# Performance work log

Measured on AMD Instinct MI355X. Metric: run time of the kernel, lower is better.

## Reference

```python
import jax, jax.numpy as jnp
import numpy as np

N_ORDER = 64
PRED_LEN = 720
SEQ_LEN = 720
ENC_IN = 321
BATCH = 16


def _hippo_legs(N):
    # HiPPO-LegS continuous transition (A, B), float64 numpy
    q = np.arange(N, dtype=np.float64)
    col, row = np.meshgrid(q, q)
    r = 2.0 * q + 1.0
    M = -(np.where(row >= col, r, 0.0) - np.diag(q))
    T = np.sqrt(np.diag(2.0 * q + 1.0))
    A = T @ M @ np.linalg.inv(T)
    B = np.diag(T)[:, None].copy()
    return A, B


def _discretize_bilinear(A, B, dt):
    # scipy.signal.cont2discrete(..., method='bilinear') equivalent
    N = A.shape[0]
    I = np.eye(N)
    BL = np.linalg.inv(I - (dt / 2.0) * A)
    Ad = BL @ (I + (dt / 2.0) * A)
    Bd = (BL @ (dt * B)).squeeze(-1)
    return Ad, Bd


def _legendre_eval_matrix(N, dt):
    # ss.eval_legendre(np.arange(N)[:,None], 1 - 2*vals).T via 3-term recurrence
    vals = np.arange(0.0, 1.0, dt)
    x = 1.0 - 2.0 * vals
    Ps = [np.ones_like(x), x]
    for n in range(1, N - 1):
        Ps.append(((2.0 * n + 1.0) * x * Ps[-1] - n * Ps[-2]) / (n + 1.0))
    return np.stack(Ps[:N], axis=0).T  # [len(vals), N]


def setup_inputs() -> dict:
    key = jax.random.key(0)
    k1, k2, k3 = jax.random.split(key, 3)
    dt = 1.0 / PRED_LEN
    A, B = _hippo_legs(N_ORDER)
    Ad, Bd = _discretize_bilinear(A, B, dt)
    eval_matrix = _legendre_eval_matrix(N_ORDER, dt)
    bound = 1.0 / np.sqrt(N_ORDER)  # torch nn.Linear default init range
    return {
        "x_enc": jax.random.normal(k1, (BATCH, SEQ_LEN, ENC_IN), dtype=jnp.float32),
        "A": jnp.asarray(Ad, dtype=jnp.float32),
        "B_vec": jnp.asarray(Bd, dtype=jnp.float32),
        "eval_matrix": jnp.asarray(eval_matrix, dtype=jnp.float32),
        "W_mlp": jax.random.uniform(k2, (N_ORDER, N_ORDER), jnp.float32, -bound, bound),
        "b_mlp": jax.random.uniform(k3, (N_ORDER,), jnp.float32, -bound, bound),
        "affine_weight": jnp.ones((1, 1, ENC_IN), jnp.float32),
        "affine_bias": jnp.zeros((1, 1, ENC_IN), jnp.float32),
    }


def reference(x_enc, A, B_vec, eval_matrix, W_mlp, b_mlp, affine_weight, affine_bias):
    P, N = eval_matrix.shape  # pred_len, proj_degree

    # RevIN-style instance normalization (means/stdev detached in torch)
    means = jax.lax.stop_gradient(jnp.mean(x_enc, axis=1, keepdims=True))
    x = x_enc - means
    stdev = jax.lax.stop_gradient(jnp.sqrt(jnp.var(x, axis=1, keepdims=True) + 1e-5))
    x = x / stdev
    x = x * affine_weight + affine_bias

    x_in = x[:, -P:]                         # [B, P, E]
    xs = jnp.transpose(x_in, (1, 0, 2))      # [P, B, E]: time-major for scan
    c0 = jnp.zeros((x_in.shape[0], x_in.shape[2], N), x_enc.dtype)

    def step(c, f):
        # c_t = c_{t-1} @ A^T + f_t B  (HiPPO-LegS linear recurrence)
        c_new = c @ A.T + f[..., None] * B_vec
        return c_new, c_new

    _, cs = jax.lax.scan(step, c0, xs)       # [P, B, E, N]

    out1 = cs @ W_mlp.T + b_mlp              # mlp over coefficient dim N
    x_dec_c = out1[P - 1]                    # [B, E, N] (seq_len >= pred_len branch)
    x_dec = x_dec_c @ eval_matrix.T          # [B, E, P] Legendre reconstruction
    x_dec = jnp.transpose(x_dec, (0, 2, 1))  # [B, P, E]

    # de-normalize
    x_dec = (x_dec - affine_bias) / (affine_weight + 1e-10)
    x_dec = x_dec * stdev + means
    return x_dec
```

## Files before the change

### kernel.cpp

```cpp
#include <hip/hip_runtime.h>
#include <math.h>

#define BATCH 16
#define SEQ   720
#define ENC   321
#define NORD  64
#define PRED  720
#define NPAIR (BATCH*ENC)

#define WS_KT    0
#define WS_EWT   (WS_KT + PRED*NORD)
#define WS_EVB   (WS_EWT + NORD*PRED)
#define WS_A64   (WS_EVB + PRED)
#define WS_KSUMP (WS_A64 + 4096)
#define WS_G     (WS_KSUMP + 17*64)
#define WS_PSUM  (WS_G + 4*96*4096)
#define WS_PSS   (WS_PSUM + 4*16*6*64)

__global__ __launch_bounds__(256, 1) void prep2(const float* __restrict__ evalm,
        const float* __restrict__ W, const float* __restrict__ bm,
        const float* __restrict__ A, const float* __restrict__ Bv,
        float* __restrict__ ws)
{
    __shared__ float dsm[12800];
    const int tid  = threadIdx.x;
    const int lane = tid & 63;
    const int wv   = tid >> 6;
    if (blockIdx.x < 12) {
        float* smW = dsm;
        float* Et  = dsm + 4160;
        const int r = blockIdx.x;
        for (int idx = tid; idx < 4096; idx += 256)
            smW[(idx>>6)*65 + (idx&63)] = W[idx];
        __syncthreads();
        float bv = bm[lane];
        #pragma unroll
        for (int k = 0; k < 15; k++) {
            int row = wv + k*4;
            int tp = r*60 + row;
            const float* ev = evalm + (size_t)tp*64;
            float acc = 0.f;
            #pragma unroll
            for (int kk = 0; kk < 16; kk++) {
                float4 e4 = *(const float4*)&ev[4*kk];
                acc += e4.x*smW[(4*kk+0)*65+lane] + e4.y*smW[(4*kk+1)*65+lane]
                     + e4.z*smW[(4*kk+2)*65+lane] + e4.w*smW[(4*kk+3)*65+lane];
            }
            Et[lane*61 + row] = acc;
            float pv = ev[lane] * bv;
            #pragma unroll
            for (int o = 32; o > 0; o >>= 1) pv += __shfl_down(pv, o);
            if (lane == 0) ws[WS_EVB + tp] = pv;
        }
        __syncthreads();
        for (int idx = tid; idx < 4096; idx += 256) {
            int m = idx >> 6, row = idx & 63;
            if (row < 60)
                ws[WS_EWT + (size_t)m*720 + r*60 + row] = Et[m*61 + row];
        }
    } else {
        float* Kl  = dsm;
        float* Ap  = dsm + 4096;
        float* ApT = dsm + 8448;
        float* Kt  = ws + WS_KT;
        for (int idx = tid; idx < 4096; idx += 256) {
            int n = idx >> 6, m = idx & 63;
            float v = A[idx];
            Ap[n*68+m] = v; ApT[m*68+n] = v;
        }
        float ksml = 0.f;
        if (tid < 64) {
            float bv = Bv[tid];
            Kl[tid] = bv;
            Kt[(size_t)719*64 + tid] = bv;
            ksml += bv;
        }
        __syncthreads();
        float ar[64];
        #pragma unroll
        for (int k = 0; k < 16; k++) {
            float4 v = *(const float4*)&Ap[lane*68 + 4*k];
            ar[4*k]=v.x; ar[4*k+1]=v.y; ar[4*k+2]=v.z; ar[4*k+3]=v.w;
        }
        for (int mm = 1; mm <= 32; mm <<= 1) {
            for (int j2 = mm + wv; j2 < 2*mm; j2 += 4) {
                const float* src = &Kl[(j2 - mm)*64];
                float acc = 0.f;
                #pragma unroll
                for (int k = 0; k < 16; k++) {
                    float4 s = *(const float4*)&src[4*k];
                    acc += ar[4*k]*s.x + ar[4*k+1]*s.y + ar[4*k+2]*s.z + ar[4*k+3]*s.w;
                }
                Kl[j2*64 + lane] = acc;
                Kt[(size_t)(719 - j2)*64 + lane] = acc;
                ksml += acc;
            }
            float nacc[16];
            #pragma unroll
            for (int q = 0; q < 16; q++) {
                int c = wv*16 + q;
                const float* src = &ApT[c*68];
                float acc = 0.f;
                #pragma unroll
                for (int k = 0; k < 16; k++) {
                    float4 s = *(const float4*)&src[4*k];
                    acc += ar[4*k]*s.x + ar[4*k+1]*s.y + ar[4*k+2]*s.z + ar[4*k+3]*s.w;
                }
                nacc[q] = acc;
            }
            __syncthreads();
            #pragma unroll
            for (int q = 0; q < 16; q++) {
                int c = wv*16 + q;
                Ap[lane*68 + c]  = nacc[q];
                ApT[c*68 + lane] = nacc[q];
            }
            __syncthreads();
            #pragma unroll
            for (int k = 0; k < 16; k++) {
                float4 v = *(const float4*)&Ap[lane*68 + 4*k];
                ar[4*k]=v.x; ar[4*k+1]=v.y; ar[4*k+2]=v.z; ar[4*k+3]=v.w;
            }
        }
        for (int idx = tid; idx < 4096; idx += 256)
            ws[WS_A64 + idx] = Ap[(idx>>6)*68 + (idx&63)];
        __syncthreads();
        Kl[wv*64 + lane] = ksml;
        __syncthreads();
        if (tid < 64)
            ws[WS_KSUMP + 16*64 + tid] = Kl[tid] + Kl[64+tid] + Kl[128+tid] + Kl[192+tid];
    }
}

__global__ __launch_bounds__(256, 1) void chains(float* __restrict__ ws)
{
    __shared__ float sv[4][64];
    __shared__ float red[4][64];
    const int tid  = threadIdx.x;
    const int lane = tid & 63;
    const int wv   = tid >> 6;
    const int r    = blockIdx.x*4 + wv;
    const float* A64 = ws + WS_A64;
    float* Kt = ws + WS_KT;
    float ar64[64];
    #pragma unroll
    for (int k = 0; k < 16; k++) {
        float4 v = *(const float4*)&A64[lane*64 + 4*k];
        ar64[4*k]=v.x; ar64[4*k+1]=v.y; ar64[4*k+2]=v.z; ar64[4*k+3]=v.w;
    }
    float ksml = 0.f;
    sv[wv][lane] = Kt[(size_t)(719 - r)*64 + lane];
    for (int j = r + 64; j <= 719; j += 64) {
        float acc = 0.f;
        #pragma unroll
        for (int k = 0; k < 16; k++) {
            float4 v = *(const float4*)&sv[wv][4*k];
            acc += ar64[4*k]*v.x + ar64[4*k+1]*v.y + ar64[4*k+2]*v.z + ar64[4*k+3]*v.w;
        }
        sv[wv][lane] = acc;
        Kt[(size_t)(719 - j)*64 + lane] = acc;
        ksml += acc;
    }
    red[wv][lane] = ksml;
    __syncthreads();
    if (tid < 64)
        ws[WS_KSUMP + blockIdx.x*64 + tid] = red[0][tid] + red[1][tid] + red[2][tid] + red[3][tid];
}

__device__ inline float4 ldx(const float* __restrict__ x, int b, int t, int e4)
{
    float4 r = make_float4(0.f,0.f,0.f,0.f);
    const float* p = x + ((size_t)b*SEQ + t)*ENC;
    if (e4 + 3 < ENC) r = *(const float4*)&p[e4];
    else {
        if (e4   < ENC) r.x = p[e4];
        if (e4+1 < ENC) r.y = p[e4+1];
        if (e4+2 < ENC) r.z = p[e4+2];
    }
    return r;
}

__global__ __launch_bounds__(256) void k2(const float* __restrict__ x,
        float* __restrict__ ws)
{
    __shared__ float xt[2][12*64];
    __shared__ float ks[2][12*64];
    __shared__ float redn[12*64];
    __shared__ float reds[12*64];
    const int tid = threadIdx.x;
    const int bid = blockIdx.x;
    const int b = bid / 24, rem = bid % 24;
    const int et = rem / 4, tsp = rem % 4;
    const int e0 = et*64, t0 = tsp*180;

    const bool xon = tid < 192;
    const bool kon = tid >= 64;
    const int sx_t  = tid >> 4;
    const int sx_e4 = (tid & 15) * 4;
    const int sk    = tid - 64;
    const int sk_t  = sk >> 4;
    const int sk_m4 = (sk & 15) * 4;

    const float* Kt = ws + WS_KT;
    float s0=0,s1=0,s2=0,s3=0, q0=0,q1=0,q2=0,q3=0;
    float4 rx = make_float4(0,0,0,0), rk = make_float4(0,0,0,0);

    if (xon) rx = ldx(x, b, t0 + sx_t, e0 + sx_e4);
    if (kon) rk = *(const float4*)&Kt[(size_t)(t0 + sk_t)*64 + sk_m4];
    if (xon) {
        *(float4*)&xt[0][sx_t*64 + sx_e4] = rx;
        s0+=rx.x; s1+=rx.y; s2+=rx.z; s3+=rx.w;
        q0+=rx.x*rx.x; q1+=rx.y*rx.y; q2+=rx.z*rx.z; q3+=rx.w*rx.w;
    }
    if (kon) *(float4*)&ks[0][sk_t*64 + sk_m4] = rk;

    const int lane = tid & 63, wv = tid >> 6;
    const int elg = lane & 15;
    const int mgr = wv*4 + (lane >> 4);
    float acc[4][4];
    #pragma unroll
    for (int j = 0; j < 4; j++)
        #pragma unroll
        for (int i = 0; i < 4; i++) acc[j][i] = 0.f;

    for (int ch = 0; ch < 15; ch++) {
        if (ch + 1 < 15) {
            if (xon) rx = ldx(x, b, t0 + (ch+1)*12 + sx_t, e0 + sx_e4);
            if (kon) rk = *(const float4*)&Kt[(size_t)(t0 + (ch+1)*12 + sk_t)*64 + sk_m4];
        }
        __syncthreads();
        const float* xb = xt[ch & 1];
        const float* kb = ks[ch & 1];
        #pragma unroll
        for (int tt = 0; tt < 12; tt++) {
            float4 f  = *(const float4*)&xb[tt*64 + elg*4];
            float4 kv = *(const float4*)&kb[tt*64 + mgr*4];
            acc[0][0]+=f.x*kv.x; acc[0][1]+=f.x*kv.y; acc[0][2]+=f.x*kv.z; acc[0][3]+=f.x*kv.w;
            acc[1][0]+=f.y*kv.x; acc[1][1]+=f.y*kv.y; acc[1][2]+=f.y*kv.z; acc[1][3]+=f.y*kv.w;
            acc[2][0]+=f.z*kv.x; acc[2][1]+=f.z*kv.y; acc[2][2]+=f.z*kv.z; acc[2][3]+=f.z*kv.w;
            acc[3][0]+=f.w*kv.x; acc[3][1]+=f.w*kv.y; acc[3][2]+=f.w*kv.z; acc[3][3]+=f.w*kv.w;
        }
        if (ch + 1 < 15) {
            if (xon) {
                *(float4*)&xt[(ch+1)&1][sx_t*64 + sx_e4] = rx;
                s0+=rx.x; s1+=rx.y; s2+=rx.z; s3+=rx.w;
                q0+=rx.x*rx.x; q1+=rx.y*rx.y; q2+=rx.z*rx.z; q3+=rx.w*rx.w;
            }
            if (kon) *(float4*)&ks[(ch+1)&1][sk_t*64 + sk_m4] = rk;
        }
    }

    float* g = ws + WS_G + (size_t)(tsp*96 + b*6 + et)*4096;
    #pragma unroll
    for (int i = 0; i < 4; i++)
        *(float4*)&g[(mgr*4 + i)*64 + elg*4] =
            make_float4(acc[0][i], acc[1][i], acc[2][i], acc[3][i]);

    __syncthreads();
    if (xon) {
        redn[sx_t*64 + sx_e4+0] = s0; redn[sx_t*64 + sx_e4+1] = s1;
        redn[sx_t*64 + sx_e4+2] = s2; redn[sx_t*64 + sx_e4+3] = s3;
        reds[sx_t*64 + sx_e4+0] = q0; reds[sx_t*64 + sx_e4+1] = q1;
        reds[sx_t*64 + sx_e4+2] = q2; reds[sx_t*64 + sx_e4+3] = q3;
    }
    __syncthreads();
    if (tid < 64) {
        float s = 0.f, q = 0.f;
        #pragma unroll
        for (int rr = 0; rr < 12; rr++) { s += redn[rr*64 + tid]; q += reds[rr*64 + tid]; }
        const size_t o = (size_t)((tsp*16 + b)*6 + et)*64 + tid;
        ws[WS_PSUM + o] = s;
        ws[WS_PSS  + o] = q;
    }
}

__global__ __launch_bounds__(256) void k3f(const float* __restrict__ aw,
        const float* __restrict__ ab, const float* __restrict__ ws,
        float* __restrict__ out)
{
    __shared__ float Cm[64*132];
    __shared__ float EWm[64*68];
    __shared__ float ssc[128], ssh[128], smean[128], ssd[128], siaw[128], sabe[128];
    __shared__ float kss[64];
    const int tid = threadIdx.x;
    const int b   = blockIdx.x / 12;
    const int rr  = blockIdx.x % 12;
    const int eT  = rr / 4;
    const int tq  = rr % 4;
    const int e0  = eT * 128;
    const int et0 = eT * 2;

    if (tid < 128) {
        const int el = tid, e = e0 + el;
        const int et = et0 + (el >> 6), eli = el & 63;
        float s = 0.f, q = 0.f;
        #pragma unroll
        for (int tsp = 0; tsp < 4; tsp++) {
            const size_t o = (size_t)((tsp*16 + b)*6 + et)*64 + eli;
            s += ws[WS_PSUM + o];
            q += ws[WS_PSS  + o];
        }
        float mean = s * (1.0f/SEQ);
        float var  = q * (1.0f/SEQ) - mean*mean;
        float sd   = sqrtf(var + 1e-5f);
        if (e < ENC) {
            float a = aw[e], av = ab[e];
            float sc = a / sd;
            ssc[el] = sc; ssh[el] = av - mean*sc;
            smean[el] = mean; ssd[el] = sd;
            siaw[el] = 1.0f/(a + 1e-10f); sabe[el] = av;
        } else {
            ssc[el]=0.f; ssh[el]=0.f; smean[el]=0.f; ssd[el]=0.f; siaw[el]=0.f; sabe[el]=0.f;
        }
    }
    if (tid < 64) {
        float s = 0.f;
        #pragma unroll
        for (int p = 0; p < 17; p++) s += ws[WS_KSUMP + p*64 + tid];
        kss[tid] = s;
    }
    __syncthreads();

    const float* G = ws + WS_G;
    #pragma unroll
    for (int k = 0; k < 8; k++) {
        int slot = k*256 + tid;
        int m = slot >> 5, el4 = (slot & 31) * 4;
        int et = et0 + (el4 >> 6), eli4 = el4 & 63;
        size_t base = (size_t)(b*6 + et)*4096 + m*64 + eli4;
        float4 g0 = *(const float4*)&G[base];
        float4 g1 = *(const float4*)&G[base + (size_t) 96*4096];
        float4 g2 = *(const float4*)&G[base + (size_t)192*4096];
        float4 g3 = *(const float4*)&G[base + (size_t)288*4096];
        float km = kss[m];
        float4 c;
        c.x = ssc[el4+0]*(g0.x+g1.x+g2.x+g3.x) + ssh[el4+0]*km;
        c.y = ssc[el4+1]*(g0.y+g1.y+g2.y+g3.y) + ssh[el4+1]*km;
        c.z = ssc[el4+2]*(g0.z+g1.z+g2.z+g3.z) + ssh[el4+2]*km;
        c.w = ssc[el4+3]*(g0.w+g1.w+g2.w+g3.w) + ssh[el4+3]*km;
        *(float4*)&Cm[m*132 + el4] = c;
    }
    __syncthreads();

    const float* EWT = ws + WS_EWT;
    const float* evb = ws + WS_EVB;
    const int tx = tid & 31;
    const int ty = tid >> 5;
    for (int ti = 0; ti < 3; ti++) {
        const int tt0 = (tq*3 + ti) * 64;
        if (ti > 0) __syncthreads();
        #pragma unroll
        for (int k = 0; k < 4; k++) {
            int slot = k*256 + tid;
            int m = slot >> 4, t4 = (slot & 15)*4;
            int tp = tt0 + t4;
            float4 v;
            if (tp + 3 < PRED) v = *(const float4*)&EWT[(size_t)m*720 + tp];
            else {
                v = make_float4(0.f,0.f,0.f,0.f);
                if (tp   < PRED) v.x = EWT[(size_t)m*720 + tp];
                if (tp+1 < PRED) v.y = EWT[(size_t)m*720 + tp+1];
                if (tp+2 < PRED) v.z = EWT[(size_t)m*720 + tp+2];
            }
            *(float4*)&EWm[m*68 + t4] = v;
        }
        __syncthreads();

        float acc[8][4];
        #pragma unroll
        for (int i = 0; i < 8; i++)
            #pragma unroll
            for (int j = 0; j < 4; j++) acc[i][j] = 0.f;

        #pragma unroll 4
        for (int m = 0; m < 64; m++) {
            float4 c4 = *(const float4*)&Cm[m*132 + tx*4];
            float4 w0 = *(const float4*)&EWm[m*68 + ty*8];
            float4 w1 = *(const float4*)&EWm[m*68 + ty*8 + 4];
            acc[0][0]+=w0.x*c4.x; acc[0][1]+=w0.x*c4.y; acc[0][2]+=w0.x*c4.z; acc[0][3]+=w0.x*c4.w;
            acc[1][0]+=w0.y*c4.x; acc[1][1]+=w0.y*c4.y; acc[1][2]+=w0.y*c4.z; acc[1][3]+=w0.y*c4.w;
            acc[2][0]+=w0.z*c4.x; acc[2][1]+=w0.z*c4.y; acc[2][2]+=w0.z*c4.z; acc[2][3]+=w0.z*c4.w;
            acc[3][0]+=w0.w*c4.x; acc[3][1]+=w0.w*c4.y; acc[3][2]+=w0.w*c4.z; acc[3][3]+=w0.w*c4.w;
            acc[4][0]+=w1.x*c4.x; acc[4][1]+=w1.x*c4.y; acc[4][2]+=w1.x*c4.z; acc[4][3]+=w1.x*c4.w;
            acc[5][0]+=w1.y*c4.x; acc[5][1]+=w1.y*c4.y; acc[5][2]+=w1.y*c4.z; acc[5][3]+=w1.y*c4.w;
            acc[6][0]+=w1.z*c4.x; acc[6][1]+=w1.z*c4.y; acc[6][2]+=w1.z*c4.z; acc[6][3]+=w1.z*c4.w;
            acc[7][0]+=w1.w*c4.x; acc[7][1]+=w1.w*c4.y; acc[7][2]+=w1.w*c4.z; acc[7][3]+=w1.w*c4.w;
        }

        const int elb = tx*4;
        const int ebase = e0 + elb;
        #pragma unroll
        for (int i = 0; i < 8; i++) {
            int tp = tt0 + ty*8 + i;
            if (tp < PRED) {
                float ev = evb[tp];
                float* op = out + ((size_t)b*PRED + tp)*ENC;
                #pragma unroll
                for (int j = 0; j < 4; j++) {
                    int e = ebase + j;
                    if (e < ENC)
                        op[e] = (acc[i][j] + ev - sabe[elb+j]) * siaw[elb+j] * ssd[elb+j]
                                + smean[elb+j];
                }
            }
        }
    }
}

extern "C" void kernel_launch(void* const* d_in, const int* in_sizes, int n_in,
                              void* d_out, int out_size, void* d_ws, size_t ws_size,
                              hipStream_t stream)
{
    const float* x     = (const float*)d_in[0];
    const float* A     = (const float*)d_in[1];
    const float* Bv    = (const float*)d_in[2];
    const float* evalm = (const float*)d_in[3];
    const float* W     = (const float*)d_in[4];
    const float* bm    = (const float*)d_in[5];
    const float* aw    = (const float*)d_in[6];
    const float* ab    = (const float*)d_in[7];
    float* ws  = (float*)d_ws;
    float* out = (float*)d_out;

    prep2 <<<13, 256, 0, stream>>>(evalm, W, bm, A, Bv, ws);
    chains<<<16, 256, 0, stream>>>(ws);
    k2    <<<BATCH*6*4, 256, 0, stream>>>(x, ws);
    k3f   <<<192, 256, 0, stream>>>(aw, ab, ws, out);
}
```

Baseline: 178.2 us.

## Rebalance Krylov power precompute: fewer matrix squarings, longer stride-16 chains

```diff
diff --git a/kernel.cpp b/kernel.cpp
--- a/kernel.cpp
+++ b/kernel.cpp
@@ -11,25 +11,130 @@
 #define WS_KT    0
 #define WS_EWT   (WS_KT + PRED*NORD)
 #define WS_EVB   (WS_EWT + NORD*PRED)
-#define WS_A64   (WS_EVB + PRED)
-#define WS_KSUMP (WS_A64 + 4096)
+#define WS_A16   (WS_EVB + PRED)
+#define WS_KSUMP (WS_A16 + 4096)
 #define WS_G     (WS_KSUMP + 17*64)
 #define WS_PSUM  (WS_G + 4*96*4096)
 #define WS_PSS   (WS_PSUM + 4*16*6*64)
 
-__global__ __launch_bounds__(256, 1) void prep2(const float* __restrict__ evalm,
-        const float* __restrict__ W, const float* __restrict__ bm,
-        const float* __restrict__ A, const float* __restrict__ Bv,
-        float* __restrict__ ws)
-{
-    __shared__ float dsm[12800];
+__global__ __launch_bounds__(256, 1) void prepK(const float* __restrict__ A,
+        const float* __restrict__ Bv, float* __restrict__ ws)
+{
+    __shared__ float Kl[16*64];
+    __shared__ float Ap[64*68];
+    __shared__ float ApT[64*68];
+    __shared__ float red[4*64];
     const int tid  = threadIdx.x;
     const int lane = tid & 63;
     const int wv   = tid >> 6;
-    if (blockIdx.x < 12) {
+    float* Kt = ws + WS_KT;
+    for (int idx = tid; idx < 4096; idx += 256) {
+        int n = idx >> 6, m = idx & 63;
+        float v = A[idx];
+        Ap[n*68+m] = v; ApT[m*68+n] = v;
+    }
+    float ksml = 0.f;
+    if (tid < 64) {
+        float bv = Bv[tid];
+        Kl[tid] = bv;
+        Kt[(size_t)719*64 + tid] = bv;
+        ksml += bv;
+    }
+    __syncthreads();
+    float ar[64];
+    #pragma unroll
+    for (int k = 0; k < 16; k++) {
+        float4 v = *(const float4*)&Ap[lane*68 + 4*k];
+        ar[4*k]=v.x; ar[4*k+1]=v.y; ar[4*k+2]=v.z; ar[4*k+3]=v.w;
+    }
+    for (int mm = 1; mm <= 8; mm <<= 1) {
+        for (int j2 = mm + wv; j2 < 2*mm; j2 += 4) {
+            const float* src = &Kl[(j2 - mm)*64];
+            float acc = 0.f;
+            #pragma unroll
+            for (int k = 0; k < 16; k++) {
+                float4 s = *(const float4*)&src[4*k];
+                acc += ar[4*k]*s.x + ar[4*k+1]*s.y + ar[4*k+2]*s.z + ar[4*k+3]*s.w;
+            }
+            Kl[j2*64 + lane] = acc;
+            Kt[(size_t)(719 - j2)*64 + lane] = acc;
+            ksml += acc;
+        }
+        float nacc[16];
+        #pragma unroll
+        for (int q = 0; q < 16; q++) {
+            int c = wv*16 + q;
+            const float* src = &ApT[c*68];
+            float acc = 0.f;
+            #pragma unroll
+            for (int k = 0; k < 16; k++) {
+                float4 s = *(const float4*)&src[4*k];
+                acc += ar[4*k]*s.x + ar[4*k+1]*s.y + ar[4*k+2]*s.z + ar[4*k+3]*s.w;
+            }
+            nacc[q] = acc;
+        }
+        __syncthreads();
+        #pragma unroll
+        for (int q = 0; q < 16; q++) {
+            int c = wv*16 + q;
+            Ap[lane*68 + c]  = nacc[q];
+            ApT[c*68 + lane] = nacc[q];
+        }
+        __syncthreads();
+        #pragma unroll
+        for (int k = 0; k < 16; k++) {
+            float4 v = *(const float4*)&Ap[lane*68 + 4*k];
+            ar[4*k]=v.x; ar[4*k+1]=v.y; ar[4*k+2]=v.z; ar[4*k+3]=v.w;
+        }
+        mm = mm;
+    }
+    for (int idx = tid; idx < 4096; idx += 256)
+        ws[WS_A16 + idx] = Ap[(idx>>6)*68 + (idx&63)];
+    __syncthreads();
+    red[wv*64 + lane] = ksml;
+    __syncthreads();
+    if (tid < 64)
+        ws[WS_KSUMP + 16*64 + tid] = red[tid] + red[64+tid] + red[128+tid] + red[192+tid];
+}
+
+__global__ __launch_bounds__(256, 1) void chainsEW(const float* __restrict__ evalm,
+        const float* __restrict__ W, const float* __restrict__ bm,
+        float* __restrict__ ws)
+{
+    __shared__ float dsm[8224];
+    const int tid  = threadIdx.x;
+    const int lane = tid & 63;
+    const int wv   = tid >> 6;
+    if (blockIdx.x < 16) {
+        if (tid >= 64) return;
+        float* sv = dsm;
+        const int r = blockIdx.x;
+        const float* A16 = ws + WS_A16;
+        float* Kt = ws + WS_KT;
+        float ar16[64];
+        #pragma unroll
+        for (int k = 0; k < 16; k++) {
+            float4 v = *(const float4*)&A16[lane*64 + 4*k];
+            ar16[4*k]=v.x; ar16[4*k+1]=v.y; ar16[4*k+2]=v.z; ar16[4*k+3]=v.w;
+        }
+        float ksml = 0.f;
+        sv[lane] = Kt[(size_t)(719 - r)*64 + lane];
+        for (int j = r + 16; j <= 719; j += 16) {
+            float acc = 0.f;
+            #pragma unroll
+            for (int k = 0; k < 16; k++) {
+                float4 v = *(const float4*)&sv[4*k];
+                acc += ar16[4*k]*v.x + ar16[4*k+1]*v.y + ar16[4*k+2]*v.z + ar16[4*k+3]*v.w;
+            }
+            sv[lane] = acc;
+            Kt[(size_t)(719 - j)*64 + lane] = acc;
+            ksml += acc;
+        }
+        ws[WS_KSUMP + r*64 + lane] = ksml;
+    } else {
         float* smW = dsm;
         float* Et  = dsm + 4160;
-        const int r = blockIdx.x;
+        const int r = blockIdx.x - 16;
         for (int idx = tid; idx < 4096; idx += 256)
             smW[(idx>>6)*65 + (idx&63)] = W[idx];
         __syncthreads();
@@ -58,113 +163,7 @@
             if (row < 60)
                 ws[WS_EWT + (size_t)m*720 + r*60 + row] = Et[m*61 + row];
         }
-    } else {
-        float* Kl  = dsm;
-        float* Ap  = dsm + 4096;
-        float* ApT = dsm + 8448;
-        float* Kt  = ws + WS_KT;
-        for (int idx = tid; idx < 4096; idx += 256) {
-            int n = idx >> 6, m = idx & 63;
-            float v = A[idx];
-            Ap[n*68+m] = v; ApT[m*68+n] = v;
-        }
-        float ksml = 0.f;
-        if (tid < 64) {
-            float bv = Bv[tid];
-            Kl[tid] = bv;
-            Kt[(size_t)719*64 + tid] = bv;
-            ksml += bv;
-        }
-        __syncthreads();
-        float ar[64];
-        #pragma unroll
-        for (int k = 0; k < 16; k++) {
-            float4 v = *(const float4*)&Ap[lane*68 + 4*k];
-            ar[4*k]=v.x; ar[4*k+1]=v.y; ar[4*k+2]=v.z; ar[4*k+3]=v.w;
-        }
-        for (int mm = 1; mm <= 32; mm <<= 1) {
-            for (int j2 = mm + wv; j2 < 2*mm; j2 += 4) {
-                const float* src = &Kl[(j2 - mm)*64];
-                float acc = 0.f;
-                #pragma unroll
-                for (int k = 0; k < 16; k++) {
-                    float4 s = *(const float4*)&src[4*k];
-                    acc += ar[4*k]*s.x + ar[4*k+1]*s.y + ar[4*k+2]*s.z + ar[4*k+3]*s.w;
-                }
-                Kl[j2*64 + lane] = acc;
-                Kt[(size_t)(719 - j2)*64 + lane] = acc;
-                ksml += acc;
-            }
-            float nacc[16];
-            #pragma unroll
-            for (int q = 0; q < 16; q++) {
-                int c = wv*16 + q;
-                const float* src = &ApT[c*68];
-                float acc = 0.f;
-                #pragma unroll
-                for (int k = 0; k < 16; k++) {
-                    float4 s = *(const float4*)&src[4*k];
-                    acc += ar[4*k]*s.x + ar[4*k+1]*s.y + ar[4*k+2]*s.z + ar[4*k+3]*s.w;
-                }
-                nacc[q] = acc;
-            }
-            __syncthreads();
-            #pragma unroll
-            for (int q = 0; q < 16; q++) {
-                int c = wv*16 + q;
-                Ap[lane*68 + c]  = nacc[q];
-                ApT[c*68 + lane] = nacc[q];
-            }
-            __syncthreads();
-            #pragma unroll
-            for (int k = 0; k < 16; k++) {
-                float4 v = *(const float4*)&Ap[lane*68 + 4*k];
-                ar[4*k]=v.x; ar[4*k+1]=v.y; ar[4*k+2]=v.z; ar[4*k+3]=v.w;
-            }
-        }
-        for (int idx = tid; idx < 4096; idx += 256)
-            ws[WS_A64 + idx] = Ap[(idx>>6)*68 + (idx&63)];
-        __syncthreads();
-        Kl[wv*64 + lane] = ksml;
-        __syncthreads();
-        if (tid < 64)
-            ws[WS_KSUMP + 16*64 + tid] = Kl[tid] + Kl[64+tid] + Kl[128+tid] + Kl[192+tid];
-    }
-}
-
-__global__ __launch_bounds__(256, 1) void chains(float* __restrict__ ws)
-{
-    __shared__ float sv[4][64];
-    __shared__ float red[4][64];
-    const int tid  = threadIdx.x;
-    const int lane = tid & 63;
-    const int wv   = tid >> 6;
-    const int r    = blockIdx.x*4 + wv;
-    const float* A64 = ws + WS_A64;
-    float* Kt = ws + WS_KT;
-    float ar64[64];
-    #pragma unroll
-    for (int k = 0; k < 16; k++) {
-        float4 v = *(const float4*)&A64[lane*64 + 4*k];
-        ar64[4*k]=v.x; ar64[4*k+1]=v.y; ar64[4*k+2]=v.z; ar64[4*k+3]=v.w;
-    }
-    float ksml = 0.f;
-    sv[wv][lane] = Kt[(size_t)(719 - r)*64 + lane];
-    for (int j = r + 64; j <= 719; j += 64) {
-        float acc = 0.f;
-        #pragma unroll
-        for (int k = 0; k < 16; k++) {
-            float4 v = *(const float4*)&sv[wv][4*k];
-            acc += ar64[4*k]*v.x + ar64[4*k+1]*v.y + ar64[4*k+2]*v.z + ar64[4*k+3]*v.w;
-        }
-        sv[wv][lane] = acc;
-        Kt[(size_t)(719 - j)*64 + lane] = acc;
-        ksml += acc;
-    }
-    red[wv][lane] = ksml;
-    __syncthreads();
-    if (tid < 64)
-        ws[WS_KSUMP + blockIdx.x*64 + tid] = red[0][tid] + red[1][tid] + red[2][tid] + red[3][tid];
+    }
 }
 
 __device__ inline float4 ldx(const float* __restrict__ x, int b, int t, int e4)
@@ -422,8 +421,8 @@
     float* ws  = (float*)d_ws;
     float* out = (float*)d_out;
 
-    prep2 <<<13, 256, 0, stream>>>(evalm, W, bm, A, Bv, ws);
-    chains<<<16, 256, 0, stream>>>(ws);
-    k2    <<<BATCH*6*4, 256, 0, stream>>>(x, ws);
-    k3f   <<<192, 256, 0, stream>>>(aw, ab, ws, out);
-}
+    prepK   <<<1, 256, 0, stream>>>(A, Bv, ws);
+    chainsEW<<<28, 256, 0, stream>>>(evalm, W, bm, ws);
+    k2      <<<BATCH*6*4, 256, 0, stream>>>(x, ws);
+    k3f     <<<192, 256, 0, stream>>>(aw, ab, ws, out);
+}
```

New measurement: 174.4 us. -2.1%, faster.
